# Kernel optimization log

Measured on AMD Instinct MI355X. Metric: run time of the kernel, lower is better.

## Reference

```python
import jax, jax.numpy as jnp
import numpy as np

B, N, D, H, L = 32, 576, 768, 8, 2
HD = D // H            # head_dim = 96
MLP = 4 * D            # 3072
GRID = 24              # sqrt(576), == max_positions
MP = 24                # max_positions
SD = 64                # spatial_dim
EPS = 1e-5


def _ln(x, g, b):
    m = jnp.mean(x, axis=-1, keepdims=True)
    v = jnp.mean((x - m) ** 2, axis=-1, keepdims=True)
    return (x - m) * jax.lax.rsqrt(v + EPS) * g + b


def setup_inputs() -> dict:
    key = jax.random.key(0)
    ks = jax.random.split(key, 16)
    s = 0.02
    inp = {
        "x": jax.random.normal(ks[0], (B, N, D), jnp.float32),
        # spatial position encoding params
        "row_embed": jax.random.normal(ks[1], (MP, SD // 2), jnp.float32) * s,
        "col_embed": jax.random.normal(ks[2], (MP, SD // 2), jnp.float32) * s,
        "pos_w": jax.random.normal(ks[3], (SD, D), jnp.float32) * s,
        "pos_b": jnp.zeros((D,), jnp.float32),
        "rel_bias": jax.random.normal(ks[4], (2 * MP - 1, 2 * MP - 1), jnp.float32) * s,
        # per-layer params, stacked on leading L axis
        "ln1_g": jnp.ones((L, D), jnp.float32),
        "ln1_b": jnp.zeros((L, D), jnp.float32),
        "ln2_g": jnp.ones((L, D), jnp.float32),
        "ln2_b": jnp.zeros((L, D), jnp.float32),
        "Wq": jax.random.normal(ks[5], (L, D, D), jnp.float32) * s,
        "bq": jnp.zeros((L, D), jnp.float32),
        "Wk": jax.random.normal(ks[6], (L, D, D), jnp.float32) * s,
        "bk": jnp.zeros((L, D), jnp.float32),
        "Wv": jax.random.normal(ks[7], (L, D, D), jnp.float32) * s,
        "bv": jnp.zeros((L, D), jnp.float32),
        "Wo": jax.random.normal(ks[8], (L, D, D), jnp.float32) * s,
        "bo": jnp.zeros((L, D), jnp.float32),
        "W1": jax.random.normal(ks[9], (L, D, MLP), jnp.float32) * s,
        "b1": jnp.zeros((L, MLP), jnp.float32),
        "W2": jax.random.normal(ks[10], (L, MLP, D), jnp.float32) * s,
        "b2": jnp.zeros((L, D), jnp.float32),
    }
    return inp


def reference(x, row_embed, col_embed, pos_w, pos_b, rel_bias,
              ln1_g, ln1_b, ln2_g, ln2_b,
              Wq, bq, Wk, bk, Wv, bv, Wo, bo,
              W1, b1, W2, b2):
    scale = HD ** -0.5

    # ---- absolute 2D position encoding (N = GRID*GRID, no CLS) ----
    pe = jnp.concatenate([
        jnp.broadcast_to(row_embed[:, None, :], (GRID, GRID, SD // 2)),
        jnp.broadcast_to(col_embed[None, :, :], (GRID, GRID, SD // 2)),
    ], axis=-1).reshape(N, SD)                      # [N, SD]
    x = x + (pe @ pos_w + pos_b)                    # broadcast over B

    # ---- relative position bias [N, N] ----
    coords = jnp.stack(jnp.meshgrid(jnp.arange(GRID), jnp.arange(GRID),
                                    indexing="ij")).reshape(2, N)  # [2, N]
    rel = coords[:, :, None] - coords[:, None, :]   # [2, N, N]
    idx = (rel[0] + MP - 1) * (2 * MP - 1) + (rel[1] + MP - 1)
    bias = rel_bias.reshape(-1)[idx]                # [N, N]

    # ---- reasoning layers ----
    for l in range(L):
        n1 = _ln(x, ln1_g[l], ln1_b[l])
        q = (n1 @ Wq[l] + bq[l]).reshape(B, N, H, HD)
        k = (n1 @ Wk[l] + bk[l]).reshape(B, N, H, HD)
        v = (n1 @ Wv[l] + bv[l]).reshape(B, N, H, HD)
        scores = jnp.einsum("bnhd,bmhd->bhnm", q, k) * scale + bias
        attn = jax.nn.softmax(scores, axis=-1)
        out = jnp.einsum("bhnm,bmhd->bnhd", attn, v).reshape(B, N, D)
        x = x + (out @ Wo[l] + bo[l])
        n2 = _ln(x, ln2_g[l], ln2_b[l])
        h = jax.nn.gelu(n2 @ W1[l] + b1[l], approximate=False)
        x = x + (h @ W2[l] + b2[l])
    return x
```

## Files before the change

### kernel.cpp

```cpp
#include <hip/hip_runtime.h>
#include <hip/hip_bf16.h>
#include <cstdint>
#include <cstddef>

typedef unsigned short u16;
using frag  = __attribute__((ext_vector_type(8))) short;
using f32x4 = __attribute__((ext_vector_type(4))) float;

#define DEV __device__ __forceinline__

DEV float bf2f(u16 u) { union { unsigned int i; float f; } x; x.i = ((unsigned int)u) << 16; return x.f; }
DEV u16 f2bf(float f) {
  union { float f; unsigned int i; } x; x.f = f;
  unsigned int r = x.i + 0x7fffu + ((x.i >> 16) & 1u);
  return (u16)(r >> 16);
}

#define MFMA16(a, b, c) __builtin_amdgcn_mfma_f32_16x16x32_bf16((a), (b), (c), 0, 0, 0)

DEV void cp16_g2l(const u16* g, u16* l) {
  __builtin_amdgcn_global_load_lds(
      reinterpret_cast<const __attribute__((address_space(1))) unsigned int*>(
          reinterpret_cast<uintptr_t>(g)),
      reinterpret_cast<__attribute__((address_space(3))) unsigned int*>(
          reinterpret_cast<uintptr_t>(l)),
      16, 0, 0);
}

template<int N> DEV void waitvm() {
  if constexpr (N == 0)      asm volatile("s_waitcnt vmcnt(0)" ::: "memory");
  else if constexpr (N == 3) asm volatile("s_waitcnt vmcnt(3)" ::: "memory");
  else if constexpr (N == 4) asm volatile("s_waitcnt vmcnt(4)" ::: "memory");
  else if constexpr (N == 6) asm volatile("s_waitcnt vmcnt(6)" ::: "memory");
  else if constexpr (N == 8) asm volatile("s_waitcnt vmcnt(8)" ::: "memory");
}

DEV void phase_barrier() {
  asm volatile("" ::: "memory");
  __builtin_amdgcn_sched_barrier(0);
  __builtin_amdgcn_s_barrier();
  __builtin_amdgcn_sched_barrier(0);
  asm volatile("" ::: "memory");
}

#define SB   32
#define SN   576
#define SD_  768
#define SH   8
#define SHD  96
#define SMLP 3072
#define BN_  (SB * SN)
#define IMG  (SN * SD_)
#define QKVS 2304

#define P_RE   0
#define P_CE   768
#define P_PW   1536
#define P_PB   50688
#define P_REL  51456
#define P_L1G  53696
#define P_L1B  55232
#define P_L2G  56768
#define P_L2B  58304
#define P_BQ   59840
#define P_BK   61376
#define P_BV   62912
#define P_BO   64448
#define P_B1   65984
#define P_B2   72128
#define P_FQB  73664
#define P_TOT  78272

__global__ void detect_kernel(const void* probe, int* flag) {
  if (threadIdx.x == 0 && blockIdx.x == 0) {
    unsigned int w = *(const unsigned int*)probe;
    flag[0] = (w == 0x3F800000u) ? 1 : 0;
  }
}

__global__ void canon_params(const void* re, const void* ce, const void* pw, const void* pb,
                             const void* rel, const void* l1g, const void* l1b,
                             const void* l2g, const void* l2b,
                             const void* pbq, const void* pbk, const void* pbv, const void* pbo,
                             const void* pb1, const void* pb2,
                             u16* __restrict__ P, const int* __restrict__ flag) {
  int i = blockIdx.x * 256 + threadIdx.x;
  const void* src; int si;
  if      (i < 768)     { src = re;  si = i; }
  else if (i < 1536)    { src = ce;  si = i - 768; }
  else if (i < 50688)   { src = pw;  si = i - 1536; }
  else if (i < 51456)   { src = pb;  si = i - 50688; }
  else if (i < 53665)   { src = rel; si = i - 51456; }
  else if (i < P_L1G)   { return; }
  else if (i < P_L1B)   { src = l1g; si = i - P_L1G; }
  else if (i < P_L2G)   { src = l1b; si = i - P_L1B; }
  else if (i < P_L2B)   { src = l2g; si = i - P_L2G; }
  else if (i < P_BQ)    { src = l2b; si = i - P_L2B; }
  else if (i < P_BK)    { src = pbq; si = i - P_BQ; }
  else if (i < P_BV)    { src = pbk; si = i - P_BK; }
  else if (i < P_BO)    { src = pbv; si = i - P_BV; }
  else if (i < P_B1)    { src = pbo; si = i - P_BO; }
  else if (i < P_B2)    { src = pb1; si = i - P_B1; }
  else if (i < P_FQB)   { src = pb2; si = i - P_B2; }
  else if (i < P_TOT) {
    int j = i - P_FQB, l = j / 2304, c = j % 2304;
    src = (c < 768) ? pbq : (c < 1536 ? pbk : pbv);
    si = l * 768 + (c % 768);
  }
  else return;
  P[i] = flag[0] ? f2bf(((const float*)src)[si]) : ((const u16*)src)[si];
}

__global__ void posenc_kernel(const u16* __restrict__ P, float* __restrict__ pe) {
  int n = blockIdx.x;
  int r = n / 24, c = n % 24;
  const u16* re = P + P_RE;
  const u16* ce = P + P_CE;
  const u16* pw = P + P_PW;
  const u16* pb = P + P_PB;
  for (int d = threadIdx.x; d < SD_; d += 256) {
    float acc = bf2f(pb[d]);
    for (int s = 0; s < 32; ++s) {
      acc += bf2f(re[r * 32 + s]) * bf2f(pw[s * SD_ + d]);
      acc += bf2f(ce[c * 32 + s]) * bf2f(pw[(32 + s) * SD_ + d]);
    }
    pe[n * SD_ + d] = acc;
  }
}

__global__ void bias_kernel(const u16* __restrict__ P, float* __restrict__ biasT) {
  int i = blockIdx.x * 256 + threadIdx.x;
  if (i < SN * SN) {
    int qi = i / SN, kj = i % SN;
    int ri = qi / 24, ci = qi % 24, rj = kj / 24, cj = kj % 24;
    int idx = (ri - rj + 23) * 47 + (ci - cj + 23);
    biasT[i] = bf2f(P[P_REL + idx]);
  }
}

__global__ void xinit_kernel(const void* __restrict__ xin, const float* __restrict__ pe,
                             float* __restrict__ X, const int* __restrict__ flag) {
  int idx = (blockIdx.x * 256 + threadIdx.x) * 4;
  int b = blockIdx.y;
  float vx, vy, vz, vw;
  if (flag[0]) {
    float4 t = *(const float4*)((const float*)xin + (size_t)b * IMG + idx);
    vx = t.x; vy = t.y; vz = t.z; vw = t.w;
  } else {
    ushort4 t = *(const ushort4*)((const u16*)xin + (size_t)b * IMG + idx);
    vx = bf2f(t.x); vy = bf2f(t.y); vz = bf2f(t.z); vw = bf2f(t.w);
  }
  float4 p = *(const float4*)(pe + idx);
  float4 o;
  o.x = vx + p.x; o.y = vy + p.y; o.z = vz + p.z; o.w = vw + p.w;
  *(float4*)(X + (size_t)b * IMG + idx) = o;
}

__global__ void transpose_any(const void* __restrict__ W, size_t eOff,
                              u16* __restrict__ Wt, int K, int N,
                              const int* __restrict__ flag) {
  __shared__ u16 tile[64][65];
  const int fp32 = flag[0];
  int n0 = blockIdx.x * 64, k0 = blockIdx.y * 64;
  int tx = threadIdx.x, ty = threadIdx.y;
#pragma unroll
  for (int j = 0; j < 16; ++j) {
    int k = ty + 4 * j;
    size_t si = eOff + (size_t)(k0 + k) * N + n0 + tx;
    tile[k][tx] = fp32 ? f2bf(((const float*)W)[si]) : ((const u16*)W)[si];
  }
  __syncthreads();
#pragma unroll
  for (int j = 0; j < 16; ++j) {
    int n = ty + 4 * j;
    Wt[(size_t)(n0 + n) * K + k0 + tx] = tile[tx][n];
  }
}

__global__ __launch_bounds__(256) void ln_kernel(const float* __restrict__ X,
                                                 const u16* __restrict__ g,
                                                 const u16* __restrict__ bb,
                                                 u16* __restrict__ Outn) {
  int row = blockIdx.x * 4 + (threadIdx.x >> 6);
  int lane = threadIdx.x & 63;
  const float* xr = X + (size_t)row * SD_;
  float4 v[3];
  float s = 0.f, sq = 0.f;
#pragma unroll
  for (int i = 0; i < 3; ++i) {
    v[i] = *(const float4*)(xr + i * 256 + lane * 4);
    s += v[i].x + v[i].y + v[i].z + v[i].w;
    sq += v[i].x * v[i].x + v[i].y * v[i].y + v[i].z * v[i].z + v[i].w * v[i].w;
  }
#pragma unroll
  for (int o = 1; o < 64; o <<= 1) {
    s += __shfl_xor(s, o, 64);
    sq += __shfl_xor(sq, o, 64);
  }
  float mean = s * (1.0f / 768.0f);
  float var = sq * (1.0f / 768.0f) - mean * mean;
  float rstd = rsqrtf(fmaxf(var, 0.f) + 1e-5f);
  u16* orow = Outn + (size_t)row * SD_;
#pragma unroll
  for (int i = 0; i < 3; ++i) {
    int d = i * 256 + lane * 4;
    ushort4 gv = *(const ushort4*)(g + d);
    ushort4 bv = *(const ushort4*)(bb + d);
    ushort4 ov;
    ov.x = f2bf((v[i].x - mean) * rstd * bf2f(gv.x) + bf2f(bv.x));
    ov.y = f2bf((v[i].y - mean) * rstd * bf2f(gv.y) + bf2f(bv.y));
    ov.z = f2bf((v[i].z - mean) * rstd * bf2f(gv.z) + bf2f(bv.z));
    ov.w = f2bf((v[i].w - mean) * rstd * bf2f(gv.w) + bf2f(bv.w));
    *(ushort4*)(orow + d) = ov;
  }
}

template<int MREP, int MODE>
__global__ __launch_bounds__(512, 2) void gemm256(
    const u16* __restrict__ A, const u16* __restrict__ Bt,
    const u16* __restrict__ bias, u16* __restrict__ Out,
    float* __restrict__ Xres, int Ncols, int K) {
  constexpr int BM = MREP * 32;
  constexpr int ASLOT = BM * 32;
  constexpr int BSLOT = 256 * 32;
  constexpr int LPT = (BM == 256) ? 4 : 3;
  __shared__ __align__(1024) u16 sA[4 * ASLOT];
  __shared__ __align__(1024) u16 sB[4 * BSLOT];

  const int tid = threadIdx.x;
  const int lane = tid & 63;
  const int w = tid >> 6;
  const int wm = w >> 2, wn = w & 3;
  const int m16 = lane & 15, q4 = lane >> 4;
  const int bn = blockIdx.x, bm = blockIdx.y;
  const int nt = K >> 5;

  const int srow = tid >> 2;
  const int kcol = (((tid & 3) ^ ((tid >> 3) & 3)) << 3);
  const u16* Ag = A + (size_t)(bm * BM + srow) * K + kcol;
  const u16* Bg = Bt + (size_t)(bn * 256 + srow) * K + kcol;
  const size_t rstep = (size_t)128 * K;
  u16* const Adst = sA + tid * 8;
  u16* const Bdst = sB + tid * 8;

  const int xk = ((q4 ^ ((m16 >> 1) & 3)) << 4);
  const char* const aBase = (const char*)sA + (((wm * (BM / 2) + m16) << 6) + xk);
  const char* const bBase = (const char*)sB + (((wn * 64 + m16) << 6) + xk);

  f32x4 acc[MREP][4] = {};

  auto stage_a = [&](int t) {
    const int s = t & 3;
    cp16_g2l(Ag + (size_t)t * 32, Adst + s * ASLOT);
    if constexpr (BM == 256) cp16_g2l(Ag + (size_t)t * 32 + rstep, Adst + s * ASLOT + 4096);
  };
  auto stage_b = [&](int t) {
    const int s = t & 3;
    cp16_g2l(Bg + (size_t)t * 32, Bdst + s * BSLOT);
    cp16_g2l(Bg + (size_t)t * 32 + rstep, Bdst + s * BSLOT + 4096);
  };

  if (nt > 0) { stage_a(0); stage_b(0); }
  if (nt > 1) { stage_a(1); stage_b(1); }
  if (nt > 2) { stage_a(2); stage_b(2); }
  if (nt > 2) waitvm<2 * LPT>(); else waitvm<0>();
  phase_barrier();

  for (int t = 0; t < nt; ++t) {
    const int s = t & 3;
    const bool st = (t + 3) < nt;
    const char* const aS = aBase + s * (ASLOT * 2);
    const char* const bS = bBase + s * (BSLOT * 2);
    frag bf[4], af[4];
#pragma unroll
    for (int j = 0; j < 4; ++j) bf[j] = *(const frag*)(bS + j * 1024);
#pragma unroll
    for (int i = 0; i < 4; ++i) af[i] = *(const frag*)(aS + i * 1024);
    if (st) stage_a(t + 3);
    if constexpr (MREP == 4) {
      if (st) stage_b(t + 3);
      if (t < nt - 3) waitvm<6>();
      else if (t == nt - 3) waitvm<3>();
      else if (t == nt - 2) waitvm<0>();
    }
    phase_barrier();
    __builtin_amdgcn_s_setprio(1);
#pragma unroll
    for (int i = 0; i < 4; ++i)
#pragma unroll
      for (int j = 0; j < 4; ++j) acc[i][j] = MFMA16(af[i], bf[j], acc[i][j]);
    __builtin_amdgcn_s_setprio(0);
    if constexpr (MREP == 8) {
      frag a2[4];
#pragma unroll
      for (int i = 0; i < 4; ++i) a2[i] = *(const frag*)(aS + 4096 + i * 1024);
      if (st) stage_b(t + 3);
      if (t < nt - 3) waitvm<8>();
      else if (t == nt - 3) waitvm<4>();
      else if (t == nt - 2) waitvm<0>();
      phase_barrier();
      __builtin_amdgcn_s_setprio(1);
#pragma unroll
      for (int i = 0; i < 4; ++i)
#pragma unroll
        for (int j = 0; j < 4; ++j) acc[4 + i][j] = MFMA16(a2[i], bf[j], acc[4 + i][j]);
      __builtin_amdgcn_s_setprio(0);
    }
  }

  const int col0 = bn * 256 + wn * 64;
  float bcol[4];
#pragma unroll
  for (int j = 0; j < 4; ++j) bcol[j] = bf2f(bias[col0 + j * 16 + m16]);

  if constexpr (MODE == 2) {
#pragma unroll
    for (int i = 0; i < MREP; ++i) {
      const int row0 = bm * BM + wm * (BM / 2) + i * 16 + q4 * 4;
#pragma unroll
      for (int j = 0; j < 4; ++j)
#pragma unroll
        for (int r = 0; r < 4; ++r)
          Xres[(size_t)(row0 + r) * Ncols + col0 + j * 16 + m16] += acc[i][j][r] + bcol[j];
    }
  } else {
    __syncthreads();
    u16* const wls = sA + w * 2048;
    const int lr = lane >> 3, lc = (lane & 7) * 8;
#pragma unroll
    for (int i = 0; i < MREP; ++i) {
#pragma unroll
      for (int j = 0; j < 4; ++j)
#pragma unroll
        for (int r = 0; r < 4; ++r) {
          float v = acc[i][j][r] + bcol[j];
          if constexpr (MODE == 1) v = 0.5f * v * (1.0f + erff(v * 0.70710678118654752f));
          wls[(q4 * 4 + r) * 72 + j * 16 + m16] = f2bf(v);
        }
      asm volatile("s_waitcnt lgkmcnt(0)" ::: "memory");
      frag o0 = *(const frag*)(wls + lr * 72 + lc);
      frag o1 = *(const frag*)(wls + (lr + 8) * 72 + lc);
      const size_t gr0 = (size_t)(bm * BM + wm * (BM / 2) + i * 16 + lr);
      *(frag*)(Out + gr0 * Ncols + col0 + lc) = o0;
      *(frag*)(Out + (gr0 + 8) * Ncols + col0 + lc) = o1;
    }
  }
}

__global__ __launch_bounds__(256) void attn_flash(const u16* __restrict__ QKV,
                                                  const float* __restrict__ biasT,
                                                  u16* __restrict__ Out, int b0) {
  __shared__ __align__(16) u16 Ks[64 * 104];
  __shared__ __align__(16) u16 Vt[96 * 72];
  __shared__ __align__(16) u16 Ps[64 * 72];
  const int tid = threadIdx.x, lane = tid & 63, w = tid >> 6;
  const int m16 = lane & 15, q4 = lane >> 4;
  const int qt = blockIdx.x, h = blockIdx.y, bl = blockIdx.z;
  const int q0 = qt * 64;
  const int row0 = bl * SN;
  const float scale = 0.10206207261596575f;

  int skey[3], soff[3];
#pragma unroll
  for (int u = 0; u < 3; ++u) { int c = tid + u * 256; skey[u] = c / 12; soff[u] = (c % 12) * 8; }

  frag aq[3];
  {
    const u16* qptr = QKV + (size_t)(row0 + q0 + w * 16 + m16) * QKVS + h * SHD;
#pragma unroll
    for (int ks = 0; ks < 3; ++ks) aq[ks] = *(const frag*)(qptr + ks * 32 + q4 * 8);
  }

  f32x4 oacc[6] = {};
  float mrun[4], lrun[4];
#pragma unroll
  for (int r = 0; r < 4; ++r) { mrun[r] = -1e30f; lrun[r] = 0.f; }

  uint4 kreg[3], vreg[3];
  auto loadKV = [&](int kt) {
#pragma unroll
    for (int u = 0; u < 3; ++u) {
      const u16* base = QKV + (size_t)(row0 + kt * 64 + skey[u]) * QKVS + h * SHD + soff[u];
      kreg[u] = *(const uint4*)(base + 768);
      vreg[u] = *(const uint4*)(base + 1536);
    }
  };
  auto writeKV = [&]() {
#pragma unroll
    for (int u = 0; u < 3; ++u) {
      *(uint4*)(Ks + skey[u] * 104 + soff[u]) = kreg[u];
      u16 tmp[8]; *(uint4*)tmp = vreg[u];
#pragma unroll
      for (int j = 0; j < 8; ++j) {
        int d = soff[u] + j;
        Vt[d * 72 + (skey[u] ^ (((d >> 3) & 7) << 3))] = tmp[j];
      }
    }
  };

  loadKV(0);
  writeKV();
  __syncthreads();

  for (int kt = 0; kt < 9; ++kt) {
    if (kt < 8) loadKV(kt + 1);

    float breg[4][4];
#pragma unroll
    for (int r = 0; r < 4; ++r) {
      const float* brow = biasT + (size_t)(q0 + w * 16 + q4 * 4 + r) * SN + kt * 64;
#pragma unroll
      for (int nt = 0; nt < 4; ++nt) breg[r][nt] = brow[nt * 16 + m16];
    }

    f32x4 sa[4];
    __builtin_amdgcn_s_setprio(1);
#pragma unroll
    for (int nt = 0; nt < 4; ++nt) {
      sa[nt] = (f32x4){0.f, 0.f, 0.f, 0.f};
#pragma unroll
      for (int ks = 0; ks < 3; ++ks) {
        frag bk = *(const frag*)(Ks + (nt * 16 + m16) * 104 + ks * 32 + q4 * 8);
        sa[nt] = MFMA16(aq[ks], bk, sa[nt]);
      }
    }
    __builtin_amdgcn_s_setprio(0);

    float sv[4][4], mnew[4];
#pragma unroll
    for (int r = 0; r < 4; ++r) {
      float mx = mrun[r];
#pragma unroll
      for (int nt = 0; nt < 4; ++nt) {
        float s = sa[nt][r] * scale + breg[r][nt];
        sv[r][nt] = s;
        mx = fmaxf(mx, s);
      }
#pragma unroll
      for (int o = 1; o < 16; o <<= 1) mx = fmaxf(mx, __shfl_xor(mx, o, 64));
      mnew[r] = mx;
    }
#pragma unroll
    for (int r = 0; r < 4; ++r) {
      float alpha = __expf(mrun[r] - mnew[r]);
      mrun[r] = mnew[r];
      float psum = 0.f;
#pragma unroll
      for (int nt = 0; nt < 4; ++nt) {
        float p = __expf(sv[r][nt] - mnew[r]);
        psum += p;
        Ps[(w * 16 + q4 * 4 + r) * 72 + nt * 16 + m16] = f2bf(p);
      }
#pragma unroll
      for (int o = 1; o < 16; o <<= 1) psum += __shfl_xor(psum, o, 64);
      lrun[r] = lrun[r] * alpha + psum;
#pragma unroll
      for (int dt = 0; dt < 6; ++dt) oacc[dt][r] *= alpha;
    }

    __builtin_amdgcn_s_setprio(1);
#pragma unroll
    for (int ch = 0; ch < 2; ++ch) {
      frag ap = *(const frag*)(Ps + (w * 16 + m16) * 72 + ch * 32 + q4 * 8);
#pragma unroll
      for (int dt = 0; dt < 6; ++dt) {
        const int d = dt * 16 + m16;
        frag bv = *(const frag*)(Vt + d * 72 + ((ch * 32 + q4 * 8) ^ (((d >> 3) & 7) << 3)));
        oacc[dt] = MFMA16(ap, bv, oacc[dt]);
      }
    }
    __builtin_amdgcn_s_setprio(0);

    if (kt < 8) {
      __syncthreads();
      writeKV();
      __syncthreads();
    }
  }

#pragma unroll
  for (int r = 0; r < 4; ++r) {
    float inv = 1.0f / lrun[r];
    size_t obase = ((size_t)((b0 + bl) * SN + q0 + w * 16 + q4 * 4 + r)) * SD_ + h * SHD;
#pragma unroll
    for (int dt = 0; dt < 6; ++dt)
      Out[obase + dt * 16 + m16] = f2bf(oacc[dt][r] * inv);
  }
}

__global__ void castout_kernel(const float* __restrict__ X, void* __restrict__ out,
                               const int* __restrict__ flag) {
  int i = (blockIdx.x * 256 + threadIdx.x) * 4;
  float4 v = *(const float4*)(X + i);
  if (flag[0]) {
    *(float4*)((float*)out + i) = v;
  } else {
    ushort4 o;
    o.x = f2bf(v.x); o.y = f2bf(v.y); o.z = f2bf(v.z); o.w = f2bf(v.w);
    *(ushort4*)((u16*)out + i) = o;
  }
}

extern "C" void kernel_launch(void* const* d_in, const int* in_sizes, int n_in,
                              void* d_out, int out_size, void* d_ws, size_t ws_size,
                              hipStream_t stream) {
  const void* x_in      = d_in[0];
  const void* row_embed = d_in[1];
  const void* col_embed = d_in[2];
  const void* pos_w     = d_in[3];
  const void* pos_b     = d_in[4];
  const void* rel_bias  = d_in[5];
  const void* ln1_g = d_in[6];
  const void* ln1_b = d_in[7];
  const void* ln2_g = d_in[8];
  const void* ln2_b = d_in[9];
  const void* Wq = d_in[10];
  const void* bq = d_in[11];
  const void* Wk = d_in[12];
  const void* bk = d_in[13];
  const void* Wv = d_in[14];
  const void* bv = d_in[15];
  const void* Wo = d_in[16];
  const void* bo = d_in[17];
  const void* W1 = d_in[18];
  const void* b1 = d_in[19];
  const void* W2 = d_in[20];
  const void* b2 = d_in[21];

  const bool tierA = ws_size >= (size_t)131000000;
  const int BC = tierA ? 16 : 8;
  const int RC = tierA ? 9216 : 4608;
  const int mR = BC * SN;
  const size_t qkvB = (size_t)mR * QKVS * 2;
  size_t bigB = qkvB;
  { size_t hB = (size_t)RC * SMLP * 2; if (hB > bigB) bigB = hB; }

  char* ws = (char*)d_ws;
  size_t off = 0;
  auto alloc = [&](size_t bytes) -> void* {
    void* p = ws + off;
    off += (bytes + 255) & ~(size_t)255;
    return p;
  };

  int*   flag = (int*)alloc(256);
  float* X    = (float*)alloc((size_t)BN_ * SD_ * 4);
  char*  big  = (char*)alloc(bigB);
  u16* QKVc = (u16*)big;
  u16* Hbuf = (u16*)big;
  float* pe    = (float*)alloc((size_t)SN * SD_ * 4);
  float* biasT = (float*)alloc((size_t)SN * SN * 4);
  u16* P     = (u16*)alloc((size_t)P_TOT * 2 + 256);
  u16* WqkvT = (u16*)alloc((size_t)QKVS * SD_ * 2);
  u16* WoT   = (u16*)alloc((size_t)SD_ * SD_ * 2);
  u16* W1T   = (u16*)alloc((size_t)SD_ * SMLP * 2);
  u16* W2T   = (u16*)alloc((size_t)SMLP * SD_ * 2);
  u16* Nfull = (u16*)d_out;

  detect_kernel<<<1, 64, 0, stream>>>(ln1_g, flag);
  canon_params<<<(P_TOT + 255) / 256, 256, 0, stream>>>(
      row_embed, col_embed, pos_w, pos_b, rel_bias,
      ln1_g, ln1_b, ln2_g, ln2_b, bq, bk, bv, bo, b1, b2, P, flag);

  posenc_kernel<<<SN, 256, 0, stream>>>(P, pe);
  bias_kernel<<<(SN * SN + 255) / 256, 256, 0, stream>>>(P, biasT);
  xinit_kernel<<<dim3(IMG / 1024, SB), 256, 0, stream>>>(x_in, pe, X, flag);

  dim3 tb(64, 4);
  for (int l = 0; l < 2; ++l) {
    const size_t wOff = (size_t)l * SD_ * SD_;
    const size_t w1Off = (size_t)l * SD_ * SMLP;
    transpose_any<<<dim3(12, 12), tb, 0, stream>>>(Wq, wOff, WqkvT, SD_, SD_, flag);
    transpose_any<<<dim3(12, 12), tb, 0, stream>>>(Wk, wOff, WqkvT + SD_ * SD_, SD_, SD_, flag);
    transpose_any<<<dim3(12, 12), tb, 0, stream>>>(Wv, wOff, WqkvT + 2 * SD_ * SD_, SD_, SD_, flag);
    transpose_any<<<dim3(12, 12), tb, 0, stream>>>(Wo, wOff, WoT, SD_, SD_, flag);
    transpose_any<<<dim3(48, 12), tb, 0, stream>>>(W1, w1Off, W1T, SD_, SMLP, flag);
    transpose_any<<<dim3(12, 48), tb, 0, stream>>>(W2, w1Off, W2T, SMLP, SD_, flag);

    ln_kernel<<<BN_ / 4, 256, 0, stream>>>(X, P + P_L1G + l * SD_, P + P_L1B + l * SD_, Nfull);

    for (int c = 0; c < SB / BC; ++c) {
      const size_t r0 = (size_t)c * mR;
      gemm256<4, 0><<<dim3(QKVS / 256, mR / 128), 512, 0, stream>>>(
          Nfull + r0 * SD_, WqkvT, P + P_FQB + l * QKVS, QKVc, nullptr, QKVS, SD_);
      attn_flash<<<dim3(SN / 64, SH, BC), 256, 0, stream>>>(QKVc, biasT, Nfull, c * BC);
    }
    gemm256<4, 2><<<dim3(SD_ / 256, BN_ / 128), 512, 0, stream>>>(
        Nfull, WoT, P + P_BO + l * SD_, nullptr, X, SD_, SD_);

    ln_kernel<<<BN_ / 4, 256, 0, stream>>>(X, P + P_L2G + l * SD_, P + P_L2B + l * SD_, Nfull);

    for (int c = 0; c < BN_ / RC; ++c) {
      const size_t r0 = (size_t)c * RC;
      gemm256<8, 1><<<dim3(SMLP / 256, RC / 256), 512, 0, stream>>>(
          Nfull + r0 * SD_, W1T, P + P_B1 + l * SMLP, Hbuf, nullptr, SMLP, SD_);
      gemm256<4, 2><<<dim3(SD_ / 256, RC / 128), 512, 0, stream>>>(
          Hbuf, W2T, P + P_B2 + l * SD_, nullptr, X + r0 * SD_, SD_, SMLP);
    }
  }

  castout_kernel<<<(size_t)BN_ * SD_ / 1024, 256, 0, stream>>>(X, d_out, flag);
}
```

Measured before the change: 1.560 ms.

## Deepen GEMM prefetch pipeline to six slots and split attention K/V loads

For the MREP==4 GEMM variant, LDS staging grows from 4 to 6 slots with a prefetch distance of 5 tiles, and vmcnt waits are adjusted to the new depth. The goal is to hide more global-load latency behind MFMA work. The flash-attention kernel gets a launch bound of 2 blocks per CU, issues V loads after the QK MFMAs, and reads bias inline instead of preloading it into registers, which lowers register pressure. The risks are lower GEMM occupancy from the larger LDS footprint and bias loads now sitting on the softmax critical path.

```diff
diff --git a/kernel.cpp b/kernel.cpp
--- a/kernel.cpp
+++ b/kernel.cpp
@@ -28,11 +28,13 @@
 }
 
 template<int N> DEV void waitvm() {
-  if constexpr (N == 0)      asm volatile("s_waitcnt vmcnt(0)" ::: "memory");
-  else if constexpr (N == 3) asm volatile("s_waitcnt vmcnt(3)" ::: "memory");
-  else if constexpr (N == 4) asm volatile("s_waitcnt vmcnt(4)" ::: "memory");
-  else if constexpr (N == 6) asm volatile("s_waitcnt vmcnt(6)" ::: "memory");
-  else if constexpr (N == 8) asm volatile("s_waitcnt vmcnt(8)" ::: "memory");
+  if constexpr (N == 0)       asm volatile("s_waitcnt vmcnt(0)" ::: "memory");
+  else if constexpr (N == 3)  asm volatile("s_waitcnt vmcnt(3)" ::: "memory");
+  else if constexpr (N == 4)  asm volatile("s_waitcnt vmcnt(4)" ::: "memory");
+  else if constexpr (N == 6)  asm volatile("s_waitcnt vmcnt(6)" ::: "memory");
+  else if constexpr (N == 8)  asm volatile("s_waitcnt vmcnt(8)" ::: "memory");
+  else if constexpr (N == 9)  asm volatile("s_waitcnt vmcnt(9)" ::: "memory");
+  else if constexpr (N == 12) asm volatile("s_waitcnt vmcnt(12)" ::: "memory");
 }
 
 DEV void phase_barrier() {
@@ -223,9 +225,10 @@
   constexpr int BM = MREP * 32;
   constexpr int ASLOT = BM * 32;
   constexpr int BSLOT = 256 * 32;
+  constexpr int SLOTS = (MREP == 4) ? 6 : 4;
   constexpr int LPT = (BM == 256) ? 4 : 3;
-  __shared__ __align__(1024) u16 sA[4 * ASLOT];
-  __shared__ __align__(1024) u16 sB[4 * BSLOT];
+  __shared__ __align__(1024) u16 sA[SLOTS * ASLOT];
+  __shared__ __align__(1024) u16 sB[SLOTS * BSLOT];
 
   const int tid = threadIdx.x;
   const int lane = tid & 63;
@@ -250,47 +253,71 @@
   f32x4 acc[MREP][4] = {};
 
   auto stage_a = [&](int t) {
-    const int s = t & 3;
+    const int s = t % SLOTS;
     cp16_g2l(Ag + (size_t)t * 32, Adst + s * ASLOT);
     if constexpr (BM == 256) cp16_g2l(Ag + (size_t)t * 32 + rstep, Adst + s * ASLOT + 4096);
   };
   auto stage_b = [&](int t) {
-    const int s = t & 3;
+    const int s = t % SLOTS;
     cp16_g2l(Bg + (size_t)t * 32, Bdst + s * BSLOT);
     cp16_g2l(Bg + (size_t)t * 32 + rstep, Bdst + s * BSLOT + 4096);
   };
 
-  if (nt > 0) { stage_a(0); stage_b(0); }
-  if (nt > 1) { stage_a(1); stage_b(1); }
-  if (nt > 2) { stage_a(2); stage_b(2); }
-  if (nt > 2) waitvm<2 * LPT>(); else waitvm<0>();
-  phase_barrier();
-
-  for (int t = 0; t < nt; ++t) {
-    const int s = t & 3;
-    const bool st = (t + 3) < nt;
-    const char* const aS = aBase + s * (ASLOT * 2);
-    const char* const bS = bBase + s * (BSLOT * 2);
-    frag bf[4], af[4];
-#pragma unroll
-    for (int j = 0; j < 4; ++j) bf[j] = *(const frag*)(bS + j * 1024);
-#pragma unroll
-    for (int i = 0; i < 4; ++i) af[i] = *(const frag*)(aS + i * 1024);
-    if (st) stage_a(t + 3);
-    if constexpr (MREP == 4) {
-      if (st) stage_b(t + 3);
-      if (t < nt - 3) waitvm<6>();
-      else if (t == nt - 3) waitvm<3>();
-      else if (t == nt - 2) waitvm<0>();
-    }
+  if constexpr (MREP == 4) {
+#pragma unroll
+    for (int p = 0; p < 5; ++p) { stage_a(p); stage_b(p); }
+    waitvm<12>();
     phase_barrier();
-    __builtin_amdgcn_s_setprio(1);
-#pragma unroll
-    for (int i = 0; i < 4; ++i)
-#pragma unroll
-      for (int j = 0; j < 4; ++j) acc[i][j] = MFMA16(af[i], bf[j], acc[i][j]);
-    __builtin_amdgcn_s_setprio(0);
-    if constexpr (MREP == 8) {
+
+    for (int t = 0; t < nt; ++t) {
+      const int s = t % SLOTS;
+      if (t + 5 < nt) { stage_a(t + 5); stage_b(t + 5); }
+      const char* const aS = aBase + (size_t)s * (ASLOT * 2);
+      const char* const bS = bBase + (size_t)s * (BSLOT * 2);
+      frag bf[4], af[4];
+#pragma unroll
+      for (int j = 0; j < 4; ++j) bf[j] = *(const frag*)(bS + j * 1024);
+#pragma unroll
+      for (int i = 0; i < 4; ++i) af[i] = *(const frag*)(aS + i * 1024);
+      const int rem = nt - 2 - t;
+      if (rem >= 4) waitvm<12>();
+      else if (rem == 3) waitvm<9>();
+      else if (rem == 2) waitvm<6>();
+      else if (rem == 1) waitvm<3>();
+      else waitvm<0>();
+      phase_barrier();
+      __builtin_amdgcn_s_setprio(1);
+#pragma unroll
+      for (int i = 0; i < 4; ++i)
+#pragma unroll
+        for (int j = 0; j < 4; ++j) acc[i][j] = MFMA16(af[i], bf[j], acc[i][j]);
+      __builtin_amdgcn_s_setprio(0);
+    }
+  } else {
+    if (nt > 0) { stage_a(0); stage_b(0); }
+    if (nt > 1) { stage_a(1); stage_b(1); }
+    if (nt > 2) { stage_a(2); stage_b(2); }
+    if (nt > 2) waitvm<2 * LPT>(); else waitvm<0>();
+    phase_barrier();
+
+    for (int t = 0; t < nt; ++t) {
+      const int s = t & 3;
+      const bool st = (t + 3) < nt;
+      const char* const aS = aBase + (size_t)s * (ASLOT * 2);
+      const char* const bS = bBase + (size_t)s * (BSLOT * 2);
+      frag bf[4], af[4];
+#pragma unroll
+      for (int j = 0; j < 4; ++j) bf[j] = *(const frag*)(bS + j * 1024);
+#pragma unroll
+      for (int i = 0; i < 4; ++i) af[i] = *(const frag*)(aS + i * 1024);
+      if (st) stage_a(t + 3);
+      phase_barrier();
+      __builtin_amdgcn_s_setprio(1);
+#pragma unroll
+      for (int i = 0; i < 4; ++i)
+#pragma unroll
+        for (int j = 0; j < 4; ++j) acc[i][j] = MFMA16(af[i], bf[j], acc[i][j]);
+      __builtin_amdgcn_s_setprio(0);
       frag a2[4];
 #pragma unroll
       for (int i = 0; i < 4; ++i) a2[i] = *(const frag*)(aS + 4096 + i * 1024);
@@ -347,9 +374,9 @@
   }
 }
 
-__global__ __launch_bounds__(256) void attn_flash(const u16* __restrict__ QKV,
-                                                  const float* __restrict__ biasT,
-                                                  u16* __restrict__ Out, int b0) {
+__global__ __launch_bounds__(256, 2) void attn_flash(const u16* __restrict__ QKV,
+                                                     const float* __restrict__ biasT,
+                                                     u16* __restrict__ Out, int b0) {
   __shared__ __align__(16) u16 Ks[64 * 104];
   __shared__ __align__(16) u16 Vt[96 * 72];
   __shared__ __align__(16) u16 Ps[64 * 72];
@@ -377,13 +404,15 @@
   for (int r = 0; r < 4; ++r) { mrun[r] = -1e30f; lrun[r] = 0.f; }
 
   uint4 kreg[3], vreg[3];
-  auto loadKV = [&](int kt) {
-#pragma unroll
-    for (int u = 0; u < 3; ++u) {
-      const u16* base = QKV + (size_t)(row0 + kt * 64 + skey[u]) * QKVS + h * SHD + soff[u];
-      kreg[u] = *(const uint4*)(base + 768);
-      vreg[u] = *(const uint4*)(base + 1536);
-    }
+  auto loadK = [&](int kt) {
+#pragma unroll
+    for (int u = 0; u < 3; ++u)
+      kreg[u] = *(const uint4*)(QKV + (size_t)(row0 + kt * 64 + skey[u]) * QKVS + 768 + h * SHD + soff[u]);
+  };
+  auto loadV = [&](int kt) {
+#pragma unroll
+    for (int u = 0; u < 3; ++u)
+      vreg[u] = *(const uint4*)(QKV + (size_t)(row0 + kt * 64 + skey[u]) * QKVS + 1536 + h * SHD + soff[u]);
   };
   auto writeKV = [&]() {
 #pragma unroll
@@ -398,20 +427,12 @@
     }
   };
 
-  loadKV(0);
+  loadK(0); loadV(0);
   writeKV();
   __syncthreads();
 
   for (int kt = 0; kt < 9; ++kt) {
-    if (kt < 8) loadKV(kt + 1);
-
-    float breg[4][4];
-#pragma unroll
-    for (int r = 0; r < 4; ++r) {
-      const float* brow = biasT + (size_t)(q0 + w * 16 + q4 * 4 + r) * SN + kt * 64;
-#pragma unroll
-      for (int nt = 0; nt < 4; ++nt) breg[r][nt] = brow[nt * 16 + m16];
-    }
+    if (kt < 8) loadK(kt + 1);
 
     f32x4 sa[4];
     __builtin_amdgcn_s_setprio(1);
@@ -426,13 +447,16 @@
     }
     __builtin_amdgcn_s_setprio(0);
 
+    if (kt < 8) loadV(kt + 1);
+
     float sv[4][4], mnew[4];
 #pragma unroll
     for (int r = 0; r < 4; ++r) {
+      const float* brow = biasT + (size_t)(q0 + w * 16 + q4 * 4 + r) * SN + kt * 64;
       float mx = mrun[r];
 #pragma unroll
       for (int nt = 0; nt < 4; ++nt) {
-        float s = sa[nt][r] * scale + breg[r][nt];
+        float s = sa[nt][r] * scale + brow[nt * 16 + m16];
         sv[r][nt] = s;
         mx = fmaxf(mx, s);
       }
```

After: 1.711 ms. 9.6% more time.
